# Kernel tuning notes

Hardware: AMD Instinct MI355X
Metric: run time of the kernel (lower is better)

The kernel has to match this reference:

```python
import jax, jax.numpy as jnp
import numpy as np

DIM = 384
HEADS = 12
WS = 7
MLPH = 1536
B = 32
EPS = 1e-5


def _rel_index():
    coords = np.stack(np.meshgrid(np.arange(WS), np.arange(WS), indexing='ij'))  # [2,7,7]
    cf = coords.reshape(2, -1)  # [2,49]
    rel = cf[:, :, None] - cf[:, None, :]  # [2,49,49]
    rel = rel.transpose(1, 2, 0).astype(np.int64)
    rel[:, :, 0] += WS - 1
    rel[:, :, 1] += WS - 1
    rel[:, :, 0] *= 2 * WS - 1
    return jnp.asarray(rel.sum(-1), dtype=jnp.int32)  # [49,49]


def setup_inputs() -> dict:
    key = jax.random.key(0)
    ks = jax.random.split(key, 16)
    H, W = 56, 56
    L = H * W
    s = 0.02
    inp = {
        'x': jax.random.normal(ks[0], (B, L, DIM), jnp.float32),
        'ln1_g': jnp.ones((DIM,), jnp.float32),
        'ln1_b': jnp.zeros((DIM,), jnp.float32),
        'qkv_w': jax.random.normal(ks[1], (DIM, 3 * DIM), jnp.float32) * s,
        'qkv_b': jnp.zeros((3 * DIM,), jnp.float32),
        'rpb_table': jax.random.normal(ks[2], ((2 * WS - 1) ** 2, HEADS), jnp.float32) * s,
        'proj_w': jax.random.normal(ks[3], (DIM, DIM), jnp.float32) * s,
        'proj_b': jnp.zeros((DIM,), jnp.float32),
        'ln2_g': jnp.ones((DIM,), jnp.float32),
        'ln2_b': jnp.zeros((DIM,), jnp.float32),
        'mlp_w1': jax.random.normal(ks[4], (DIM, MLPH), jnp.float32) * s,
        'mlp_b1': jnp.zeros((MLPH,), jnp.float32),
        'mlp_w2': jax.random.normal(ks[5], (MLPH, DIM), jnp.float32) * s,
        'mlp_b2': jnp.zeros((DIM,), jnp.float32),
        'rel_idx': _rel_index(),
        'H': H,
        'W': W,
    }
    return inp


def _ln(x, g, b):
    m = jnp.mean(x, axis=-1, keepdims=True)
    v = jnp.mean(jnp.square(x - m), axis=-1, keepdims=True)
    return (x - m) * jax.lax.rsqrt(v + EPS) * g + b


def reference(x, ln1_g, ln1_b, qkv_w, qkv_b, rpb_table, proj_w, proj_b,
              ln2_g, ln2_b, mlp_w1, mlp_b1, mlp_w2, mlp_b2, rel_idx, H, W):
    Bb, L, C = x.shape
    N = WS * WS
    hd = C // HEADS
    scale = hd ** -0.5

    shortcut = x
    h = _ln(x, ln1_g, ln1_b).reshape(Bb, H, W, C)
    # window partition -> [nW, 49, C]
    h = h.reshape(Bb, H // WS, WS, W // WS, WS, C).transpose(0, 1, 3, 2, 4, 5)
    wins = h.reshape(-1, N, C)
    nW = wins.shape[0]

    qkv = (wins @ qkv_w + qkv_b).reshape(nW, N, 3, HEADS, hd).transpose(2, 0, 3, 1, 4)
    q, k, v = qkv[0] * scale, qkv[1], qkv[2]  # [nW, heads, 49, hd]

    attn = jnp.einsum('bhnd,bhmd->bhnm', q, k)
    bias = rpb_table[rel_idx].transpose(2, 0, 1)  # [heads,49,49]
    attn = jax.nn.softmax(attn + bias[None], axis=-1)
    out = jnp.einsum('bhnm,bhmd->bhnd', attn, v).transpose(0, 2, 1, 3).reshape(nW, N, C)
    out = out @ proj_w + proj_b

    # window reverse -> [B, L, C]
    out = out.reshape(Bb, H // WS, W // WS, WS, WS, C).transpose(0, 1, 3, 2, 4, 5).reshape(Bb, L, C)

    x = shortcut + out
    h2 = _ln(x, ln2_g, ln2_b)
    mlp = jax.nn.gelu(h2 @ mlp_w1 + mlp_b1, approximate=False) @ mlp_w2 + mlp_b2
    return x + mlp
```

## Files before the change

### kernel.cpp

```cpp
#include <hip/hip_runtime.h>
#include <hip/hip_bf16.h>
#include <cstdint>
#include <cstddef>

#define HEADS 12
#define LL 3136
#define ROWS 100352
#define SCALE 0.17677669529663687f

typedef __hip_bfloat16 bf16;
typedef __attribute__((ext_vector_type(8))) short short8;
typedef __attribute__((ext_vector_type(4))) short s4;
typedef __attribute__((ext_vector_type(4))) float f32x4;

__device__ __forceinline__ float bf2f(unsigned short u) {
  union { uint32_t u32; float f; } x; x.u32 = ((uint32_t)u) << 16; return x.f;
}
__device__ __forceinline__ unsigned short f2bf_bits(float f) {
  union { float f; uint32_t u; } x; x.f = f;
  uint32_t r = x.u + 0x7fffu + ((x.u >> 16) & 1u);
  return (unsigned short)(r >> 16);
}

__global__ __launch_bounds__(64) void prep_fragB(const float* __restrict__ src,
    bf16* __restrict__ dst, int K, int N, int scaleLim, float scale) {
  const int nf = blockIdx.x, kf = blockIdx.y;
  const int l = threadIdx.x;
  const int n = nf * 16 + (l & 15);
  const int k0 = kf * 32 + (l >> 4) * 8;
  const float sc = (n < scaleLim) ? scale : 1.f;
  short8 v;
  #pragma unroll
  for (int j = 0; j < 8; ++j)
    v[j] = (short)f2bf_bits(src[(size_t)(k0 + j) * N + n] * sc);
  *(short8*)&dst[(((size_t)nf * (K >> 5) + kf) * 64 + l) * 8] = v;
}

__global__ void prep_qb(const float* __restrict__ qkv_b, float* __restrict__ qb) {
  int idx = blockIdx.x * 256 + threadIdx.x;
  if (idx < 1152) qb[idx] = qkv_b[idx] * (idx < 384 ? SCALE : 1.0f);
}

__global__ void prep_biasM(const float* __restrict__ rpb, const int* __restrict__ rel,
                           f32x4* __restrict__ biasM) {
  int h = blockIdx.x;
  int t = blockIdx.y;
  int mi = t >> 2, ni = t & 3;
  int lane = threadIdx.x;
  int q = ni * 16 + (lane & 15);
  int g = lane >> 4;
  f32x4 v;
  #pragma unroll
  for (int j = 0; j < 4; ++j) {
    int k = mi * 16 + g * 4 + j;
    float b;
    if (k < 49) b = (q < 49) ? rpb[rel[q * 49 + k] * HEADS + h] : 0.f;
    else        b = -1e30f;
    v[j] = b;
  }
  biasM[((h * 4 + mi) * 4 + ni) * 64 + lane] = v;
}

template<bool WIN, bool BF16IN>
__global__ __launch_bounds__(256) void ln_kernel(const float* __restrict__ xf,
    const bf16* __restrict__ xb, const float* __restrict__ g,
    const float* __restrict__ b, bf16* __restrict__ out) {
  int row = blockIdx.x * 4 + (threadIdx.x >> 6);
  int lane = threadIdx.x & 63;
  size_t src;
  if (WIN) {
    int w = row / 49, p = row - w * 49;
    int bb = w >> 6, wy = (w >> 3) & 7, wx = w & 7;
    int iy = p / 7, ix = p - iy * 7;
    int l = (wy * 7 + iy) * 56 + wx * 7 + ix;
    src = ((size_t)bb * LL + l) * 384;
  } else {
    src = (size_t)row * 384;
  }
  float vals[6];
  float s = 0.f, s2 = 0.f;
  #pragma unroll
  for (int j = 0; j < 6; ++j) {
    float v = BF16IN ? bf2f(*(const unsigned short*)&xb[src + lane + 64 * j])
                     : xf[src + lane + 64 * j];
    vals[j] = v; s += v; s2 += v * v;
  }
  #pragma unroll
  for (int off = 32; off >= 1; off >>= 1) {
    s  += __shfl_xor(s, off);
    s2 += __shfl_xor(s2, off);
  }
  float m  = s * (1.f / 384.f);
  float var = s2 * (1.f / 384.f) - m * m;
  float rs = rsqrtf(var + 1e-5f);
  bf16* orow = out + (size_t)row * 384;
  #pragma unroll
  for (int j = 0; j < 6; ++j) {
    int c = lane + 64 * j;
    orow[c] = __float2bfloat16((vals[j] - m) * rs * g[c] + b[c]);
  }
}

template<int EPI>
__global__ __launch_bounds__(256) void gemm_bt(const bf16* __restrict__ A,
    const bf16* __restrict__ Bt, const float* __restrict__ bias,
    bf16* __restrict__ Cb, float* __restrict__ Cf, const float* __restrict__ resid,
    const bf16* __restrict__ residb, int M, int N, int K) {
  __shared__ bf16 lsA[3][128 * 32];
  const int t = threadIdx.x;
  const int lane = t & 63;
  const int wave = t >> 6;
  const int wm = wave >> 1, wn = wave & 1;
  const int lrow = lane & 15;
  const int lk = (lane >> 4) * 8;
  const int nbx = N >> 7;
  const int nwg = (M >> 7) * nbx;
  const int cpx = nwg >> 3;
  const int id2 = (blockIdx.x & 7) * cpx + (blockIdx.x >> 3);
  const int n0 = (id2 % nbx) * 128;
  const int m0 = (id2 / nbx) * 128;
  const int nkf = K >> 5;

  f32x4 acc[4][4];
  #pragma unroll
  for (int i = 0; i < 4; ++i)
    #pragma unroll
    for (int j = 0; j < 4; ++j) acc[i][j] = (f32x4){0.f, 0.f, 0.f, 0.f};

  auto stageA = [&](int buf, int tile) {
    int k0 = tile * 32;
    #pragma unroll
    for (int i = 0; i < 2; ++i) {
      int e = (i * 256 + t) * 8;
      int r = e >> 5, c = e & 31;
      const bf16* ga = A + (size_t)(m0 + r) * K + (k0 + c);
      __builtin_amdgcn_global_load_lds((const __attribute__((address_space(1))) void*)ga,
          (__attribute__((address_space(3))) void*)&lsA[buf][e], 16, 0, 0);
    }
  };

  auto loadB = [&](int kf, short8 (&dst)[4]) {
    const bf16* fb = Bt + (((size_t)((n0 >> 4) + wn * 4) * nkf + kf) * 64 + lane) * 8;
    #pragma unroll
    for (int ni = 0; ni < 4; ++ni)
      dst[ni] = *(const short8*)(fb + (size_t)ni * nkf * 512);
  };

  auto computeA = [&](int buf, const short8 (&bfr)[4]) {
    short8 af[4];
    #pragma unroll
    for (int mi = 0; mi < 4; ++mi)
      af[mi] = *(const short8*)&lsA[buf][(wm * 64 + mi * 16 + lrow) * 32 + lk];
    __builtin_amdgcn_s_setprio(1);
    #pragma unroll
    for (int mi = 0; mi < 4; ++mi)
      #pragma unroll
      for (int ni = 0; ni < 4; ++ni)
        acc[mi][ni] = __builtin_amdgcn_mfma_f32_16x16x32_bf16(af[mi], bfr[ni], acc[mi][ni], 0, 0, 0);
    __builtin_amdgcn_s_setprio(0);
  };

  const int nt = K >> 5;
  short8 b0[4], b1[4];
  stageA(0, 0);
  loadB(0, b0);
  stageA(1, 1);
  int cur = 0;
  for (int it = 0; it < nt; it += 2) {
    {
      __builtin_amdgcn_s_barrier();
      if (it + 1 < nt) loadB(it + 1, b1);
      if (it + 2 < nt) stageA((cur + 2) % 3, it + 2);
      int rem = nt - 1 - it;
      if (rem >= 2)      asm volatile("s_waitcnt vmcnt(12)" ::: "memory");
      else if (rem == 1) asm volatile("s_waitcnt vmcnt(10)" ::: "memory");
      else               asm volatile("s_waitcnt vmcnt(4)"  ::: "memory");
      __builtin_amdgcn_s_barrier();
      computeA(cur, b0);
      cur = (cur == 2) ? 0 : cur + 1;
    }
    if (it + 1 < nt) {
      __builtin_amdgcn_s_barrier();
      if (it + 2 < nt) loadB(it + 2, b0);
      if (it + 3 < nt) stageA((cur + 2) % 3, it + 3);
      int rem = nt - 2 - it;
      if (rem >= 2)      asm volatile("s_waitcnt vmcnt(12)" ::: "memory");
      else if (rem == 1) asm volatile("s_waitcnt vmcnt(10)" ::: "memory");
      else               asm volatile("s_waitcnt vmcnt(4)"  ::: "memory");
      __builtin_amdgcn_s_barrier();
      computeA(cur, b1);
      cur = (cur == 2) ? 0 : cur + 1;
    }
  }

  #pragma unroll
  for (int mi = 0; mi < 4; ++mi) {
    #pragma unroll
    for (int ni = 0; ni < 4; ++ni) {
      int col = n0 + wn * 64 + ni * 16 + lrow;
      float bv = bias[col];
      #pragma unroll
      for (int j = 0; j < 4; ++j) {
        int row = m0 + wm * 64 + mi * 16 + (lane >> 4) * 4 + j;
        float v = acc[mi][ni][j] + bv;
        if constexpr (EPI == 0) {
          Cb[(size_t)row * N + col] = __float2bfloat16(v);
        } else if constexpr (EPI == 1) {
          v = v * 0.5f * (1.0f + erff(v * 0.70710678118654752f));
          Cb[(size_t)row * N + col] = __float2bfloat16(v);
        } else if constexpr (EPI == 2) {
          int w = row / 49, p = row - w * 49;
          int bb = w >> 6, wy = (w >> 3) & 7, wx = w & 7;
          int iy = p / 7, ix = p - iy * 7;
          int l = (wy * 7 + iy) * 56 + wx * 7 + ix;
          size_t di = ((size_t)bb * LL + l) * 384 + col;
          Cb[di] = __float2bfloat16(v + resid[di]);
        } else {
          size_t di = (size_t)row * N + col;
          Cf[di] = v + bf2f(*(const unsigned short*)&residb[di]);
        }
      }
    }
  }
}

__global__ __launch_bounds__(256) void attn_mfma(const bf16* __restrict__ qkv,
    const f32x4* __restrict__ biasM, bf16* __restrict__ out) {
  __shared__ __align__(16) short lds4[4][6272];
  const int wv = threadIdx.x >> 6;
  const int lane = threadIdx.x & 63;
  const int w = blockIdx.x * 4 + wv;
  const int h = blockIdx.y;
  short* L = &lds4[wv][0];
  const short* base = (const short*)(qkv + (size_t)w * 49 * 1152 + h * 32);

  #pragma unroll
  for (int i = 0; i < 4; ++i) {
    int t = i * 64 + lane;
    int r = t >> 2, c = t & 3;
    short8 qv, kv, vv;
    if (r < 49) {
      const short* rp = base + (size_t)r * 1152;
      qv = *(const short8*)(rp + c * 8);
      kv = *(const short8*)(rp + 384 + c * 8);
      vv = *(const short8*)(rp + 768 + c * 8);
    } else {
      qv = (short8)0; kv = (short8)0; vv = (short8)0;
    }
    *(short8*)&L[r * 32 + c * 8] = kv;
    *(short8*)&L[2048 + r * 32 + c * 8] = qv;
    #pragma unroll
    for (int j = 0; j < 8; ++j) L[4096 + (c * 8 + j) * 68 + r] = vv[j];
  }

  const int g = lane >> 4, r15 = lane & 15;

  short8 ka[4], qb[4];
  #pragma unroll
  for (int mi = 0; mi < 4; ++mi)
    ka[mi] = *(const short8*)&L[(mi * 16 + r15) * 32 + g * 8];
  #pragma unroll
  for (int ni = 0; ni < 4; ++ni)
    qb[ni] = *(const short8*)&L[2048 + (ni * 16 + r15) * 32 + g * 8];

  f32x4 sT[4][4];
  #pragma unroll
  for (int mi = 0; mi < 4; ++mi)
    #pragma unroll
    for (int ni = 0; ni < 4; ++ni)
      sT[mi][ni] = biasM[((h * 4 + mi) * 4 + ni) * 64 + lane];
  #pragma unroll
  for (int mi = 0; mi < 4; ++mi)
    #pragma unroll
    for (int ni = 0; ni < 4; ++ni)
      sT[mi][ni] = __builtin_amdgcn_mfma_f32_16x16x32_bf16(ka[mi], qb[ni], sT[mi][ni], 0, 0, 0);

  float inv_[4];
  #pragma unroll
  for (int ni = 0; ni < 4; ++ni) {
    float m = -1e30f;
    #pragma unroll
    for (int mi = 0; mi < 4; ++mi)
      #pragma unroll
      for (int j = 0; j < 4; ++j) m = fmaxf(m, sT[mi][ni][j]);
    m = fmaxf(m, __shfl_xor(m, 16));
    m = fmaxf(m, __shfl_xor(m, 32));
    float s = 0.f;
    #pragma unroll
    for (int mi = 0; mi < 4; ++mi)
      #pragma unroll
      for (int j = 0; j < 4; ++j) {
        float p = __expf(sT[mi][ni][j] - m);
        sT[mi][ni][j] = p; s += p;
      }
    s += __shfl_xor(s, 16);
    s += __shfl_xor(s, 32);
    inv_[ni] = 1.f / s;
  }

  s4 pa[4][4];
  #pragma unroll
  for (int mi = 0; mi < 4; ++mi)
    #pragma unroll
    for (int ni = 0; ni < 4; ++ni) {
      s4 p;
      #pragma unroll
      for (int j = 0; j < 4; ++j)
        p[j] = (short)f2bf_bits(sT[mi][ni][j] * inv_[ni]);
      pa[mi][ni] = p;
    }

  s4 vb[4][2];
  #pragma unroll
  for (int mi = 0; mi < 4; ++mi)
    #pragma unroll
    for (int di = 0; di < 2; ++di)
      vb[mi][di] = *(const s4*)&L[4096 + (di * 16 + r15) * 68 + mi * 16 + g * 4];

  f32x4 o[4][2];
  #pragma unroll
  for (int ni = 0; ni < 4; ++ni)
    #pragma unroll
    for (int di = 0; di < 2; ++di) o[ni][di] = (f32x4){0.f, 0.f, 0.f, 0.f};

  asm volatile("s_nop 3" ::: );
  #pragma unroll
  for (int ni = 0; ni < 4; ++ni)
    #pragma unroll
    for (int di = 0; di < 2; ++di)
      #pragma unroll
      for (int mi = 0; mi < 4; ++mi) {
#if __has_builtin(__builtin_amdgcn_mfma_f32_16x16x16bf16_1k)
        o[ni][di] = __builtin_amdgcn_mfma_f32_16x16x16bf16_1k(pa[mi][ni], vb[mi][di], o[ni][di], 0, 0, 0);
#else
        asm volatile("v_mfma_f32_16x16x16_bf16 %0, %1, %2, %0"
                     : "+v"(o[ni][di]) : "v"(pa[mi][ni]), "v"(vb[mi][di]));
#endif
      }
  asm volatile("s_nop 7\n\ts_nop 7" ::: );

  bf16* op = out + ((size_t)w * 49) * 384 + h * 32;
  #pragma unroll
  for (int ni = 0; ni < 4; ++ni)
    #pragma unroll
    for (int di = 0; di < 2; ++di)
      #pragma unroll
      for (int j = 0; j < 4; ++j) {
        int q = ni * 16 + g * 4 + j;
        if (q < 49)
          op[(size_t)q * 384 + di * 16 + r15] = __float2bfloat16(o[ni][di][j]);
      }
}

extern "C" void kernel_launch(void* const* d_in, const int* in_sizes, int n_in,
                              void* d_out, int out_size, void* d_ws, size_t ws_size,
                              hipStream_t stream) {
  const float* x      = (const float*)d_in[0];
  const float* ln1_g  = (const float*)d_in[1];
  const float* ln1_b  = (const float*)d_in[2];
  const float* qkv_w  = (const float*)d_in[3];
  const float* qkv_b  = (const float*)d_in[4];
  const float* rpb    = (const float*)d_in[5];
  const float* proj_w = (const float*)d_in[6];
  const float* proj_b = (const float*)d_in[7];
  const float* ln2_g  = (const float*)d_in[8];
  const float* ln2_b  = (const float*)d_in[9];
  const float* mlp_w1 = (const float*)d_in[10];
  const float* mlp_b1 = (const float*)d_in[11];
  const float* mlp_w2 = (const float*)d_in[12];
  const float* mlp_b2 = (const float*)d_in[13];
  const int*   rel    = (const int*)d_in[14];

  char* ws = (char*)d_ws;
  const size_t OFF_WQKV  = 0;
  const size_t OFF_WPROJ = OFF_WQKV + (size_t)1152 * 384 * 2;
  const size_t OFF_WM1   = OFF_WPROJ + (size_t)384 * 384 * 2;
  const size_t OFF_WM2   = OFF_WM1 + (size_t)1536 * 384 * 2;
  const size_t OFF_QB    = OFF_WM2 + (size_t)384 * 1536 * 2;
  const size_t OFF_HWIN  = 3659776;
  const size_t OFF_QKV   = OFF_HWIN + (size_t)ROWS * 384 * 2;
  const size_t OFF_ATTN  = OFF_QKV + (size_t)ROWS * 1152 * 2;
  const size_t OFF_X2    = OFF_ATTN + (size_t)ROWS * 384 * 2;
  const size_t OFF_M1    = OFF_QKV;
  const size_t OFF_H2    = OFF_HWIN;
  const size_t OFF_BIASM = OFF_X2 + (size_t)ROWS * 384 * 2;

  bf16*  wqkv  = (bf16*)(ws + OFF_WQKV);
  bf16*  wproj = (bf16*)(ws + OFF_WPROJ);
  bf16*  wm1   = (bf16*)(ws + OFF_WM1);
  bf16*  wm2   = (bf16*)(ws + OFF_WM2);
  float* qb    = (float*)(ws + OFF_QB);
  f32x4* biasM = (f32x4*)(ws + OFF_BIASM);
  bf16*  hwin  = (bf16*)(ws + OFF_HWIN);
  bf16*  qkvb  = (bf16*)(ws + OFF_QKV);
  bf16*  attnb = (bf16*)(ws + OFF_ATTN);
  bf16*  x2b   = (bf16*)(ws + OFF_X2);
  bf16*  m1    = (bf16*)(ws + OFF_M1);
  bf16*  h2    = (bf16*)(ws + OFF_H2);
  float* outp  = (float*)d_out;

  prep_fragB<<<dim3(1152 / 16, 384 / 32), 64, 0, stream>>>(qkv_w, wqkv, 384, 1152, 384, SCALE);
  prep_fragB<<<dim3(384 / 16, 384 / 32), 64, 0, stream>>>(proj_w, wproj, 384, 384, 0, 1.f);
  prep_fragB<<<dim3(1536 / 16, 384 / 32), 64, 0, stream>>>(mlp_w1, wm1, 384, 1536, 0, 1.f);
  prep_fragB<<<dim3(384 / 16, 1536 / 32), 64, 0, stream>>>(mlp_w2, wm2, 1536, 384, 0, 1.f);
  prep_qb<<<5, 256, 0, stream>>>(qkv_b, qb);
  prep_biasM<<<dim3(12, 16), 64, 0, stream>>>(rpb, rel, biasM);

  ln_kernel<true, false><<<ROWS / 4, 256, 0, stream>>>(x, nullptr, ln1_g, ln1_b, hwin);
  gemm_bt<0><<<(1152 / 128) * (ROWS / 128), 256, 0, stream>>>(
      hwin, wqkv, qb, qkvb, nullptr, nullptr, nullptr, ROWS, 1152, 384);
  attn_mfma<<<dim3(512, HEADS), 256, 0, stream>>>(qkvb, biasM, attnb);
  gemm_bt<2><<<(384 / 128) * (ROWS / 128), 256, 0, stream>>>(
      attnb, wproj, proj_b, x2b, nullptr, x, nullptr, ROWS, 384, 384);
  ln_kernel<false, true><<<ROWS / 4, 256, 0, stream>>>(nullptr, x2b, ln2_g, ln2_b, h2);
  gemm_bt<1><<<(1536 / 128) * (ROWS / 128), 256, 0, stream>>>(
      h2, wm1, mlp_b1, m1, nullptr, nullptr, nullptr, ROWS, 1536, 384);
  gemm_bt<3><<<(384 / 128) * (ROWS / 128), 256, 0, stream>>>(
      m1, wm2, mlp_b2, nullptr, outp, nullptr, x2b, ROWS, 384, 1536);
}
```

Before: 972.3 us.

## Simplify GEMM to double-buffered LDS pipeline and use tanh-form GELU

Replaces the triple-buffered A staging, which had hand-tuned vmcnt waits, split barriers and raised wave priority around the MFMAs, with a plain double buffer. Each k-step now ends in a full __syncthreads, and the B fragments are copied register to register. It also swaps the exact erf GELU in the MLP epilogue for a tanh-style approximation written with an exponential, to cut the epilogue's transcendental cost. The cost is less overlap between memory and MFMA work, a full barrier on every iteration, and small numerical differences from the exact GELU the reference uses.

```diff
diff --git a/kernel.cpp b/kernel.cpp
--- a/kernel.cpp
+++ b/kernel.cpp
@@ -20,6 +20,11 @@
   union { float f; uint32_t u; } x; x.f = f;
   uint32_t r = x.u + 0x7fffu + ((x.u >> 16) & 1u);
   return (unsigned short)(r >> 16);
+}
+__device__ __forceinline__ float gelu_fast(float x) {
+  float t2 = x * (1.5957691216f + 0.0713548162726f * x * x);
+  float e = __expf(t2);
+  return x * (e / (e + 1.0f) );
 }
 
 __global__ __launch_bounds__(64) void prep_fragB(const float* __restrict__ src,
@@ -106,7 +111,7 @@
     const bf16* __restrict__ Bt, const float* __restrict__ bias,
     bf16* __restrict__ Cb, float* __restrict__ Cf, const float* __restrict__ resid,
     const bf16* __restrict__ residb, int M, int N, int K) {
-  __shared__ bf16 lsA[3][128 * 32];
+  __shared__ bf16 lsA[2][128 * 32];
   const int t = threadIdx.x;
   const int lane = t & 63;
   const int wave = t >> 6;
@@ -151,46 +156,31 @@
     #pragma unroll
     for (int mi = 0; mi < 4; ++mi)
       af[mi] = *(const short8*)&lsA[buf][(wm * 64 + mi * 16 + lrow) * 32 + lk];
-    __builtin_amdgcn_s_setprio(1);
     #pragma unroll
     for (int mi = 0; mi < 4; ++mi)
       #pragma unroll
       for (int ni = 0; ni < 4; ++ni)
         acc[mi][ni] = __builtin_amdgcn_mfma_f32_16x16x32_bf16(af[mi], bfr[ni], acc[mi][ni], 0, 0, 0);
-    __builtin_amdgcn_s_setprio(0);
   };
 
   const int nt = K >> 5;
   short8 b0[4], b1[4];
   stageA(0, 0);
   loadB(0, b0);
-  stageA(1, 1);
+  __syncthreads();
   int cur = 0;
-  for (int it = 0; it < nt; it += 2) {
-    {
-      __builtin_amdgcn_s_barrier();
-      if (it + 1 < nt) loadB(it + 1, b1);
-      if (it + 2 < nt) stageA((cur + 2) % 3, it + 2);
-      int rem = nt - 1 - it;
-      if (rem >= 2)      asm volatile("s_waitcnt vmcnt(12)" ::: "memory");
-      else if (rem == 1) asm volatile("s_waitcnt vmcnt(10)" ::: "memory");
-      else               asm volatile("s_waitcnt vmcnt(4)"  ::: "memory");
-      __builtin_amdgcn_s_barrier();
-      computeA(cur, b0);
-      cur = (cur == 2) ? 0 : cur + 1;
-    }
+  for (int it = 0; it < nt; ++it) {
     if (it + 1 < nt) {
-      __builtin_amdgcn_s_barrier();
-      if (it + 2 < nt) loadB(it + 2, b0);
-      if (it + 3 < nt) stageA((cur + 2) % 3, it + 3);
-      int rem = nt - 2 - it;
-      if (rem >= 2)      asm volatile("s_waitcnt vmcnt(12)" ::: "memory");
-      else if (rem == 1) asm volatile("s_waitcnt vmcnt(10)" ::: "memory");
-      else               asm volatile("s_waitcnt vmcnt(4)"  ::: "memory");
-      __builtin_amdgcn_s_barrier();
-      computeA(cur, b1);
-      cur = (cur == 2) ? 0 : cur + 1;
-    }
+      stageA(cur ^ 1, it + 1);
+      loadB(it + 1, b1);
+    }
+    computeA(cur, b0);
+    __syncthreads();
+    if (it + 1 < nt) {
+      #pragma unroll
+      for (int i = 0; i < 4; ++i) b0[i] = b1[i];
+    }
+    cur ^= 1;
   }
 
   #pragma unroll
@@ -206,8 +196,7 @@
         if constexpr (EPI == 0) {
           Cb[(size_t)row * N + col] = __float2bfloat16(v);
         } else if constexpr (EPI == 1) {
-          v = v * 0.5f * (1.0f + erff(v * 0.70710678118654752f));
-          Cb[(size_t)row * N + col] = __float2bfloat16(v);
+          Cb[(size_t)row * N + col] = __float2bfloat16(gelu_fast(v));
         } else if constexpr (EPI == 2) {
           int w = row / 49, p = row - w * 49;
           int bb = w >> 6, wy = (w >> 3) & 7, wx = w & 7;
```

Result: faster. 938.3 us (-3.5%).
